# Optimization experiments

Hardware: AMD Instinct MI355X
Metric: run time of the kernel (lower is better)

## Reference

```python
import jax, jax.numpy as jnp
import numpy as np

D = 64      # hidden_dim
H = 4       # num_attention_heads
DH = D // H # head_dim
B = 64      # graphs per batch
SCALE = np.float32(np.sqrt(DH))


def _sage(x, edge, wl, bl, wr):
    # SAGEConv: lin_l(mean_j x_j) + lin_r(x_i); mean over incoming edges (dst = edge[1])
    src, dst = edge[0], edge[1]
    n = x.shape[0]
    agg = jax.ops.segment_sum(x[src], dst, num_segments=n)
    cnt = jax.ops.segment_sum(jnp.ones((edge.shape[1],), x.dtype), dst, num_segments=n)
    mean = agg / jnp.maximum(cnt, 1.0)[:, None]
    return mean @ wl + bl + x @ wr


def _cross_attn(xq, xk, w, b):
    # w: [3, D, D] stacked (Q, K, V) projections; b: [3, D]
    Q = (xq @ w[0] + b[0]).reshape(-1, H, DH)  # [Nq, H, DH]
    K = (xk @ w[1] + b[1]).reshape(-1, H, DH)  # [Nk, H, DH]
    V = (xk @ w[2] + b[2]).reshape(-1, H, DH)
    scores = jnp.einsum('qhd,khd->hqk', Q, K) / SCALE  # [H, Nq, Nk]
    wgt = jax.nn.softmax(scores, axis=-1)
    out = jnp.einsum('hqk,khd->qhd', wgt, V)
    return out.reshape(xq.shape[0], D)


def _segment_mean(x, seg, num):
    s = jax.ops.segment_sum(x, seg, num_segments=num)
    c = jax.ops.segment_sum(jnp.ones((x.shape[0],), x.dtype), seg, num_segments=num)
    return s / jnp.maximum(c, 1.0)[:, None]


def setup_inputs() -> dict:
    key = jax.random.key(0)
    ks = jax.random.split(key, 32)
    N_MOL, N_PROT, E_MOL, E_PROT = 2048, 8192, 32768, 131072
    MOL_IN, PROT_IN = 32, 64

    def lin(k, i, o, s=None):
        s = 1.0 / np.sqrt(i) if s is None else s
        return (jax.random.normal(k, (i, o), jnp.float32) * s)

    inp = {
        'x_mol': jax.random.normal(ks[0], (N_MOL, MOL_IN), jnp.float32),
        'x_prot': jax.random.normal(ks[1], (N_PROT, PROT_IN), jnp.float32),
        'm1_wl': lin(ks[2], MOL_IN, D), 'm1_bl': jnp.zeros((D,), jnp.float32), 'm1_wr': lin(ks[3], MOL_IN, D),
        'm2_wl': lin(ks[4], D, D), 'm2_bl': jnp.zeros((D,), jnp.float32), 'm2_wr': lin(ks[5], D, D),
        'p1_wl': lin(ks[6], PROT_IN, D), 'p1_bl': jnp.zeros((D,), jnp.float32), 'p1_wr': lin(ks[7], PROT_IN, D),
        'p2_wl': lin(ks[8], D, D), 'p2_bl': jnp.zeros((D,), jnp.float32), 'p2_wr': lin(ks[9], D, D),
        'amp_w': jax.random.normal(ks[10], (3, D, D), jnp.float32) / np.sqrt(D),
        'amp_b': jnp.zeros((3, D), jnp.float32),
        'apm_w': jax.random.normal(ks[11], (3, D, D), jnp.float32) / np.sqrt(D),
        'apm_b': jnp.zeros((3, D), jnp.float32),
        'fc1_w': lin(ks[12], 2 * D, D), 'fc1_b': jnp.zeros((D,), jnp.float32),
        'fc2_w': lin(ks[13], D, 1), 'fc2_b': jnp.zeros((1,), jnp.float32),
        'edge_mol': jax.random.randint(ks[14], (2, E_MOL), 0, N_MOL, jnp.int32),
        'edge_prot': jax.random.randint(ks[15], (2, E_PROT), 0, N_PROT, jnp.int32),
        'batch_mol': jnp.sort(jax.random.randint(ks[16], (N_MOL,), 0, B, jnp.int32)),
        'batch_prot': jnp.sort(jax.random.randint(ks[17], (N_PROT,), 0, B, jnp.int32)),
    }
    return inp


def reference(x_mol, x_prot,
              m1_wl, m1_bl, m1_wr, m2_wl, m2_bl, m2_wr,
              p1_wl, p1_bl, p1_wr, p2_wl, p2_bl, p2_wr,
              amp_w, amp_b, apm_w, apm_b,
              fc1_w, fc1_b, fc2_w, fc2_b,
              edge_mol, edge_prot, batch_mol, batch_prot):
    # two SAGE conv blocks per graph, ReLU after each (HeteroConv with one edge type)
    h_mol = jax.nn.relu(_sage(x_mol, edge_mol, m1_wl, m1_bl, m1_wr))
    h_mol = jax.nn.relu(_sage(h_mol, edge_mol, m2_wl, m2_bl, m2_wr))
    h_prot = jax.nn.relu(_sage(x_prot, edge_prot, p1_wl, p1_bl, p1_wr))
    h_prot = jax.nn.relu(_sage(h_prot, edge_prot, p2_wl, p2_bl, p2_wr))
    # cross attention (mol queries prot, prot queries mol) + residual
    h_mol_c = h_mol + _cross_attn(h_mol, h_prot, amp_w, amp_b)
    h_prot_c = h_prot + _cross_attn(h_prot, h_mol, apm_w, apm_b)
    # global mean pool per graph
    z_mol = _segment_mean(h_mol_c, batch_mol, B)    # [B, D]
    z_prot = _segment_mean(h_prot_c, batch_prot, B)  # [B, D]
    z = jnp.concatenate([z_mol, z_prot], axis=1)     # [B, 2D]
    x = jax.nn.relu(z @ fc1_w + fc1_b)
    out = jax.nn.sigmoid(x @ fc2_w + fc2_b)
    return out.squeeze(-1)  # [B]
```

## Files before the change

kernel.cpp:

```cpp
#include <hip/hip_runtime.h>
#include <math.h>

#define D 64
#define NB 64

typedef __attribute__((ext_vector_type(8))) short bf16x8;
typedef __attribute__((ext_vector_type(4))) float f32x4;
typedef __attribute__((ext_vector_type(16))) float f32x16;

#define M3(a, b, c) fmaxf(fmaxf((a), (b)), (c))

__device__ __forceinline__ unsigned short f2bf(float f) {
    unsigned u = __float_as_uint(f);
    u += 0x7FFF + ((u >> 16) & 1);
    return (unsigned short)(u >> 16);
}
__device__ __forceinline__ unsigned pk_bf16(float lo, float hi) {
    unsigned r;
    asm("v_cvt_pk_bf16_f32 %0, %1, %2" : "=v"(r) : "v"(lo), "v"(hi));
    return r;
}
__device__ __forceinline__ float fexp2(float x) {
    float r;
    asm("v_exp_f32 %0, %1" : "=v"(r) : "v"(x));
    return r;
}

__global__ void k_prep2(const int* __restrict__ em, int Em,
                        const int* __restrict__ ep, int Ep,
                        int* __restrict__ degm, int* __restrict__ degp,
                        const int* __restrict__ bm, int Nm, int* __restrict__ bsM,
                        const int* __restrict__ bp, int Np, int* __restrict__ bsP) {
    int i = blockIdx.x * blockDim.x + threadIdx.x;
    if (i < Em) atomicAdd(&degm[em[Em + i]], 1);
    int j = i - Em;
    if (j >= 0 && j < Ep) atomicAdd(&degp[ep[Ep + j]], 1);
    if (i < Nm) {
        int cur = bm[i];
        int prev = (i == 0) ? -1 : bm[i - 1];
        for (int b = prev + 1; b <= cur; ++b) bsM[b] = i;
        if (i == Nm - 1)
            for (int b = cur + 1; b <= NB; ++b) bsM[b] = Nm;
    }
    int j2 = i - Nm;
    if (j2 >= 0 && j2 < Np) {
        int cur = bp[j2];
        int prev = (j2 == 0) ? -1 : bp[j2 - 1];
        for (int b = prev + 1; b <= cur; ++b) bsP[b] = j2;
        if (j2 == Np - 1)
            for (int b = cur + 1; b <= NB; ++b) bsP[b] = Np;
    }
}

__global__ __launch_bounds__(256) void k_scan2(
        const int* __restrict__ degm, int Nm, int* __restrict__ rpm, int* __restrict__ curm,
        const int* __restrict__ degp, int Np, int* __restrict__ rpp, int* __restrict__ curp) {
    __shared__ int sdeg[8192];
    __shared__ int chunk[256];
    const int* deg = blockIdx.x ? degp : degm;
    int N = blockIdx.x ? Np : Nm;
    int* rowptr = blockIdx.x ? rpp : rpm;
    int* cursor = blockIdx.x ? curp : curm;
    int t = threadIdx.x;
    for (int i = t; i < N; i += 256) sdeg[i] = deg[i];
    __syncthreads();
    int C = (N + 255) / 256;
    int start = t * C;
    int sum = 0;
    for (int i = 0; i < C; ++i)
        if (start + i < N) sum += sdeg[start + i];
    chunk[t] = sum;
    __syncthreads();
    for (int ofs = 1; ofs < 256; ofs <<= 1) {
        int v = (t >= ofs) ? chunk[t - ofs] : 0;
        __syncthreads();
        chunk[t] += v;
        __syncthreads();
    }
    int base = (t == 0) ? 0 : chunk[t - 1];
    for (int i = 0; i < C && start + i < N; ++i) {
        rowptr[start + i] = base;
        cursor[start + i] = base;
        base += sdeg[start + i];
    }
    if (t == 255) rowptr[N] = base;
}

__global__ void k_scatter2(const int* __restrict__ em, int Em, int* __restrict__ curm,
                           int* __restrict__ csrm,
                           const int* __restrict__ ep, int Ep, int* __restrict__ curp,
                           int* __restrict__ csrp) {
    int i = blockIdx.x * blockDim.x + threadIdx.x;
    if (i < Em) {
        int s = em[i], d = em[Em + i];
        csrm[atomicAdd(&curm[d], 1)] = s;
    }
    int j = i - Em;
    if (j >= 0 && j < Ep) {
        int s = ep[j], d = ep[Ep + j];
        csrp[atomicAdd(&curp[d], 1)] = s;
    }
}

template<int FIN>
__device__ __forceinline__ void gsage_body(
        const float* __restrict__ x, const int* __restrict__ rowptr,
        const int* __restrict__ csr, int N,
        const float* __restrict__ wl, const float* __restrict__ bl,
        const float* __restrict__ wr, float* __restrict__ out,
        int blk, float* __restrict__ swl, float* __restrict__ swr,
        float* __restrict__ sagg, float* __restrict__ sx) {
    for (int i = threadIdx.x; i < FIN * D; i += 256) { swl[i] = wl[i]; swr[i] = wr[i]; }
    int w = threadIdx.x >> 6;
    int lane = threadIdx.x & 63;
    int r = blk * 4 + w;
    if (r < N) {
        int e0 = rowptr[r], e1 = rowptr[r + 1];
        float inv = 1.0f / fmaxf((float)(e1 - e0), 1.0f);
        if (FIN == 64) {
            float a0 = 0.f, a1 = 0.f, a2 = 0.f, a3 = 0.f;
            int e = e0;
            for (; e + 3 < e1; e += 4) {
                a0 += x[(size_t)csr[e] * FIN + lane];
                a1 += x[(size_t)csr[e + 1] * FIN + lane];
                a2 += x[(size_t)csr[e + 2] * FIN + lane];
                a3 += x[(size_t)csr[e + 3] * FIN + lane];
            }
            for (; e < e1; ++e) a0 += x[(size_t)csr[e] * FIN + lane];
            sagg[w * 64 + lane] = ((a0 + a1) + (a2 + a3)) * inv;
            sx[w * 64 + lane] = x[(size_t)r * FIN + lane];
        } else {
            int f = lane & 31, half = lane >> 5;
            float a = 0.f;
            for (int e = e0 + half; e < e1; e += 2)
                a += x[(size_t)csr[e] * FIN + f];
            a += __shfl_xor(a, 32);
            if (half == 0) {
                sagg[w * 64 + f] = a * inv;
                sx[w * 64 + f] = x[(size_t)r * FIN + f];
            }
        }
    }
    __syncthreads();
    if (r >= N) return;
    int c = lane;
    float acc = bl[c];
    #pragma unroll 8
    for (int k = 0; k < FIN; ++k) {
        acc += sagg[w * 64 + k] * swl[k * D + c];
        acc += sx[w * 64 + k] * swr[k * D + c];
    }
    out[(size_t)r * D + c] = fmaxf(acc, 0.0f);
}

template<int FA, int FB>
__global__ __launch_bounds__(256) void k_gsage2(
        const float* __restrict__ xA, const int* __restrict__ rpA,
        const int* __restrict__ csrA, int NA,
        const float* __restrict__ wlA, const float* __restrict__ blA,
        const float* __restrict__ wrA, float* __restrict__ outA,
        const float* __restrict__ xB, const int* __restrict__ rpB,
        const int* __restrict__ csrB, int NB_,
        const float* __restrict__ wlB, const float* __restrict__ blB,
        const float* __restrict__ wrB, float* __restrict__ outB) {
    __shared__ float swl[64 * 64];
    __shared__ float swr[64 * 64];
    __shared__ float sagg[4 * 64];
    __shared__ float sx[4 * 64];
    int bA = NA / 4;
    if ((int)blockIdx.x < bA)
        gsage_body<FA>(xA, rpA, csrA, NA, wlA, blA, wrA, outA, blockIdx.x, swl, swr, sagg, sx);
    else
        gsage_body<FB>(xB, rpB, csrB, NB_, wlB, blB, wrB, outB, blockIdx.x - bA, swl, swr, sagg, sx);
}

__global__ __launch_bounds__(256) void k_qkv2(
        const float* __restrict__ xA, int NA, const float* __restrict__ xB, int NB_,
        const float* __restrict__ amp_w, const float* __restrict__ amp_b,
        const float* __restrict__ apm_w, const float* __restrict__ apm_b, float qs,
        unsigned short* __restrict__ QA, unsigned short* __restrict__ KA, unsigned short* __restrict__ VA,
        unsigned short* __restrict__ QB, unsigned short* __restrict__ KB, unsigned short* __restrict__ VB) {
    __shared__ float sq[D * D], sk[D * D], sv[D * D], sx[16 * D];
    int bA = NA / 16;
    const float *x, *wq, *bq, *wk, *bk, *wv, *bv;
    unsigned short *oq, *ok, *ov;
    int blk;
    if ((int)blockIdx.x < bA) {
        x = xA; blk = blockIdx.x;
        wq = amp_w;        bq = amp_b;
        wk = apm_w + 4096; bk = apm_b + 64;
        wv = apm_w + 8192; bv = apm_b + 128;
        oq = QA; ok = KA; ov = VA;
    } else {
        x = xB; blk = blockIdx.x - bA;
        wq = apm_w;        bq = apm_b;
        wk = amp_w + 4096; bk = amp_b + 64;
        wv = amp_w + 8192; bv = amp_b + 128;
        oq = QB; ok = KB; ov = VB;
    }
    for (int i = threadIdx.x; i < D * D; i += 256) { sq[i] = wq[i]; sk[i] = wk[i]; sv[i] = wv[i]; }
    int rbase = blk * 16;
    for (int i = threadIdx.x; i < 16 * D; i += 256) sx[i] = x[(size_t)rbase * D + i];
    __syncthreads();
    int c = threadIdx.x & 63;
    int r0 = (threadIdx.x >> 6) * 4;
    for (int rr = 0; rr < 4; ++rr) {
        int r = r0 + rr;
        float aq = bq[c], ak = bk[c], av = bv[c];
        #pragma unroll 8
        for (int k = 0; k < D; ++k) {
            float xv = sx[r * D + k];
            aq += xv * sq[k * D + c];
            ak += xv * sk[k * D + c];
            av += xv * sv[k * D + c];
        }
        size_t o = (size_t)(rbase + r) * D + c;
        oq[o] = f2bf(aq * qs);
        ok[o] = f2bf(ak);
        ov[o] = f2bf(av);
    }
}

__global__ void k_transp2(const unsigned short* __restrict__ inM, unsigned short* __restrict__ outM, int Nm,
                          const unsigned short* __restrict__ inP, unsigned short* __restrict__ outP, int Np) {
    __shared__ unsigned short tile[64][72];
    int bm = Nm >> 6;
    const unsigned short* in; unsigned short* out; int N;
    int blk = blockIdx.x;
    if (blk < bm) { in = inM; out = outM; N = Nm; }
    else { blk -= bm; in = inP; out = outP; N = Np; }
    int t = threadIdx.x;
    int rbase = blk * 64;
    {
        int r = t >> 2, c0 = (t & 3) * 16;
        const uint4* src = (const uint4*)(in + (size_t)(rbase + r) * 64 + c0);
        uint4 a = src[0], b = src[1];
        *(uint4*)(&tile[r][c0]) = a;
        *(uint4*)(&tile[r][c0 + 8]) = b;
    }
    __syncthreads();
    {
        int c = t >> 2, r0 = (t & 3) * 16;
        union { uint2 v2[4]; unsigned short s[16]; } u;
        #pragma unroll
        for (int i = 0; i < 16; ++i) u.s[i] = tile[r0 + i][c];
        int key0 = rbase + r0;
        int kc = key0 & ~31;
        int b16 = key0 & 16;
        unsigned short* op = out + (size_t)c * N;
        const int gmap[4] = {0, 8, 4, 12};
        #pragma unroll
        for (int b = 0; b < 4; ++b)
            *(uint2*)(op + kc + b16 + gmap[b]) = u.v2[b];
    }
    if (t < 8) {
        uint4 ones;
        ones.x = ones.y = ones.z = ones.w = 0x3F803F80u;
        *(uint4*)(out + (size_t)64 * N + rbase + t * 8) = ones;
    }
}

#define MAXTREE(cm, s0, s1)                                                   \
    {                                                                         \
        float c0 = M3(s0[0], s0[1], s0[2]);                                   \
        float c1 = M3(s0[3], s0[4], s0[5]);                                   \
        float c2 = M3(s0[6], s0[7], s0[8]);                                   \
        float c3 = M3(s0[9], s0[10], s0[11]);                                 \
        float c4 = M3(s0[12], s0[13], s0[14]);                                \
        float c5 = M3(s0[15], s1[0], s1[1]);                                  \
        float c6 = M3(s1[2], s1[3], s1[4]);                                   \
        float c7 = M3(s1[5], s1[6], s1[7]);                                   \
        float c8 = M3(s1[8], s1[9], s1[10]);                                  \
        float c9 = M3(s1[11], s1[12], s1[13]);                                \
        float ca = fmaxf(s1[14], s1[15]);                                     \
        float d0 = M3(c0, c1, c2);                                            \
        float d1 = M3(c3, c4, c5);                                            \
        float d2 = M3(c6, c7, c8);                                            \
        float d3 = M3(c9, ca, d0);                                            \
        cm = M3(d1, d2, d3);                                                  \
    }

#define PVPACK(S, KB)                                                         \
    {                                                                         \
        union { unsigned u[4]; bf16x8 v; } f1, f2;                            \
        f1.u[0] = pk_bf16((S)[0], (S)[1]);   f1.u[1] = pk_bf16((S)[2], (S)[3]);  \
        f1.u[2] = pk_bf16((S)[4], (S)[5]);   f1.u[3] = pk_bf16((S)[6], (S)[7]);  \
        f2.u[0] = pk_bf16((S)[8], (S)[9]);   f2.u[1] = pk_bf16((S)[10], (S)[11]);\
        f2.u[2] = pk_bf16((S)[12], (S)[13]); f2.u[3] = pk_bf16((S)[14], (S)[15]);\
        bf16x8 vb0 = *(const bf16x8*)(vbase + (KB) + half * 8);               \
        bf16x8 vb1 = *(const bf16x8*)(vbase + (KB) + 16 + half * 8);          \
        __builtin_amdgcn_s_setprio(1);                                        \
        o = __builtin_amdgcn_mfma_f32_32x32x16_bf16(f1.v, vb0, o, 0, 0, 0);   \
        o = __builtin_amdgcn_mfma_f32_32x32x16_bf16(f2.v, vb1, o, 0, 0, 0);   \
        __builtin_amdgcn_s_setprio(0);                                        \
    }

__global__ __launch_bounds__(256) void k_attn5(
        const unsigned short* __restrict__ QmB, const unsigned short* __restrict__ KpB,
        const unsigned short* __restrict__ VpT, int Nm, int Np, int lsm,
        float* __restrict__ poM, float* __restrict__ pmM, float* __restrict__ plM,
        const unsigned short* __restrict__ QpB, const unsigned short* __restrict__ KmB,
        const unsigned short* __restrict__ VmT, int lsp,
        float* __restrict__ poP, float* __restrict__ pmP, float* __restrict__ plP) {
    const unsigned short *Q, *K, *Vt;
    int Nq, Nk, ls;
    float *po, *pm, *pl;
    if (blockIdx.y == 0) { Q = QmB; K = KpB; Vt = VpT; Nq = Nm; Nk = Np; ls = lsm; po = poM; pm = pmM; pl = plM; }
    else                 { Q = QpB; K = KmB; Vt = VmT; Nq = Np; Nk = Nm; ls = lsp; po = poP; pm = pmP; pl = plP; }
    int nqt = Nq >> 5;
    if ((int)blockIdx.x >= (nqt << ls)) return;
    const int qt = blockIdx.x >> ls;
    const int split = blockIdx.x & ((1 << ls) - 1);
    const int kchunk = Nk >> ls;
    const int h = threadIdx.x >> 6;
    const int lane = threadIdx.x & 63;
    const int cq = lane & 31;
    const int half = lane >> 5;
    const int h16 = h * 16;

    bf16x8 qb = *(const bf16x8*)(Q + ((size_t)(qt * 32 + cq) * D + h16 + half * 8));
    int drow = (cq < 16) ? (h16 + cq) : (cq == 16 ? 64 : h16 + 15);
    const unsigned short* vbase = Vt + (size_t)drow * Nk;

    f32x16 o, mC;
    #pragma unroll
    for (int i = 0; i < 16; ++i) { o[i] = 0.f; mC[i] = 0.f; }
    float m;

    const int kstart = split * kchunk;
    {
        const int kb = kstart;
        bf16x8 ka0 = *(const bf16x8*)(K + ((size_t)(kb + cq) * D + h16 + half * 8));
        bf16x8 ka1 = *(const bf16x8*)(K + ((size_t)(kb + 32 + cq) * D + h16 + half * 8));
        f32x16 s0 = __builtin_amdgcn_mfma_f32_32x32x16_bf16(ka0, qb, mC, 0, 0, 0);
        f32x16 s1 = __builtin_amdgcn_mfma_f32_32x32x16_bf16(ka1, qb, mC, 0, 0, 0);
        float cm;
        MAXTREE(cm, s0, s1);
        #pragma unroll
        for (int off = 1; off < 64; off <<= 1) cm = fmaxf(cm, __shfl_xor(cm, off));
        m = cm;
        #pragma unroll
        for (int i = 0; i < 16; ++i) {
            s0[i] = fexp2(s0[i] - m);
            s1[i] = fexp2(s1[i] - m);
            mC[i] = -m;
        }
        PVPACK(s0, kb)
        PVPACK(s1, kb + 32)
    }
    #pragma unroll 2
    for (int kb = kstart + 64; kb < kstart + kchunk; kb += 32) {
        bf16x8 ka = *(const bf16x8*)(K + ((size_t)(kb + cq) * D + h16 + half * 8));
        f32x16 s = __builtin_amdgcn_mfma_f32_32x32x16_bf16(ka, qb, mC, 0, 0, 0);
        #pragma unroll
        for (int i = 0; i < 16; ++i) s[i] = fexp2(s[i]);
        PVPACK(s, kb)
    }

    size_t pbase = (size_t)split * Nq + qt * 32;
    if (half == 0)
        pm[(pbase + cq) * 4 + h] = m;
    if (cq == 16) {
        #pragma unroll
        for (int r = 0; r < 16; ++r) {
            int qr = (r & 3) + 8 * (r >> 2) + 4 * half;
            pl[(pbase + qr) * 4 + h] = o[r];
        }
    }
    if (cq < 16) {
        #pragma unroll
        for (int r = 0; r < 16; ++r) {
            int qr = (r & 3) + 8 * (r >> 2) + 4 * half;
            po[(pbase + qr) * 64 + h16 + cq] = o[r];
        }
    }
}

template<int NS>
__device__ __forceinline__ void comb_body(
        const float* __restrict__ po, const float* __restrict__ pm,
        const float* __restrict__ pl, int Nq,
        const float* __restrict__ resid, float* __restrict__ outc, int i) {
    int q = i >> 4;
    int part = i & 15;
    int d0 = part * 4;
    int h = part >> 2;
    float pmv[NS], plv[NS];
    #pragma unroll
    for (int s = 0; s < NS; ++s) pmv[s] = pm[((size_t)s * Nq + q) * 4 + h];
    #pragma unroll
    for (int s = 0; s < NS; ++s) plv[s] = pl[((size_t)s * Nq + q) * 4 + h];
    float M = pmv[0];
    #pragma unroll
    for (int s = 1; s < NS; ++s) M = fmaxf(M, pmv[s]);
    float4 O = {0.f, 0.f, 0.f, 0.f};
    float L = 0.f;
    #pragma unroll
    for (int s = 0; s < NS; ++s) {
        float wgt = fexp2(pmv[s] - M);
        float4 pv = *(const float4*)(po + ((size_t)s * Nq + q) * 64 + d0);
        O.x += pv.x * wgt; O.y += pv.y * wgt; O.z += pv.z * wgt; O.w += pv.w * wgt;
        L += plv[s] * wgt;
    }
    float invL = 1.0f / L;
    float4 rv = *(const float4*)(resid + (size_t)q * 64 + d0);
    float4 res;
    res.x = rv.x + O.x * invL;
    res.y = rv.y + O.y * invL;
    res.z = rv.z + O.z * invL;
    res.w = rv.w + O.w * invL;
    *(float4*)(outc + (size_t)q * 64 + d0) = res;
}

template<int NSM, int NSP>
__global__ void k_comb2t(
        const float* __restrict__ poM, const float* __restrict__ pmM, const float* __restrict__ plM,
        int Nm, const float* __restrict__ residM, float* __restrict__ outM,
        const float* __restrict__ poP, const float* __restrict__ pmP, const float* __restrict__ plP,
        int Np, const float* __restrict__ residP, float* __restrict__ outP) {
    int idx = blockIdx.x * blockDim.x + threadIdx.x;
    int mtot = Nm * 16;
    if (idx < mtot)
        comb_body<NSM>(poM, pmM, plM, Nm, residM, outM, idx);
    else if (idx - mtot < Np * 16)
        comb_body<NSP>(poP, pmP, plP, Np, residP, outP, idx - mtot);
}

__global__ void k_comb2(
        const float* __restrict__ poM, const float* __restrict__ pmM, const float* __restrict__ plM,
        int nsM, int Nm, const float* __restrict__ residM, float* __restrict__ outM,
        const float* __restrict__ poP, const float* __restrict__ pmP, const float* __restrict__ plP,
        int nsP, int Np, const float* __restrict__ residP, float* __restrict__ outP) {
    int idx = blockIdx.x * blockDim.x + threadIdx.x;
    const float *po, *pm, *pl, *resid;
    float* outc;
    int ns, Nq, i;
    int mtot = Nm * 64;
    if (idx < mtot) {
        po = poM; pm = pmM; pl = plM; ns = nsM; Nq = Nm; resid = residM; outc = outM; i = idx;
    } else {
        i = idx - mtot;
        if (i >= Np * 64) return;
        po = poP; pm = pmP; pl = plP; ns = nsP; Nq = Np; resid = residP; outc = outP;
    }
    int q = i >> 6, d = i & 63, h = d >> 4;
    float M = -1e30f;
    for (int s = 0; s < ns; ++s)
        M = fmaxf(M, pm[((size_t)s * Nq + q) * 4 + h]);
    float O = 0.f, L = 0.f;
    for (int s = 0; s < ns; ++s) {
        float wgt = fexp2(pm[((size_t)s * Nq + q) * 4 + h] - M);
        O += po[((size_t)s * Nq + q) * 64 + d] * wgt;
        L += pl[((size_t)s * Nq + q) * 4 + h] * wgt;
    }
    outc[i] = resid[i] + O / L;
}

__global__ __launch_bounds__(256) void k_pool2(
        const float* __restrict__ hM, const int* __restrict__ bsM,
        const float* __restrict__ hP, const int* __restrict__ bsP,
        float* __restrict__ zsum, float* __restrict__ zcnt) {
    __shared__ float red[4][64];
    int b = blockIdx.x & 63;
    int isP = blockIdx.x >> 6;
    const float* h = isP ? hP : hM;
    const int* bs = isP ? bsP : bsM;
    int colOff = isP ? 64 : 0;
    int n0 = bs[b], n1 = bs[b + 1];
    int w = threadIdx.x >> 6, c = threadIdx.x & 63;
    float acc = 0.f;
    for (int n = n0 + w; n < n1; n += 4)
        acc += h[(size_t)n * 64 + c];
    red[w][c] = acc;
    __syncthreads();
    if (w == 0) {
        float s = (red[0][c] + red[1][c]) + (red[2][c] + red[3][c]);
        zsum[b * 128 + colOff + c] = s;
        if (c == 0) zcnt[b * 2 + isP] = (float)(n1 - n0);
    }
}

__global__ __launch_bounds__(256) void k_head2(
        const float* __restrict__ zsum, const float* __restrict__ zcnt,
        const float* __restrict__ fc1w, const float* __restrict__ fc1b,
        const float* __restrict__ fc2w, const float* __restrict__ fc2b,
        float* __restrict__ out) {
    int b = blockIdx.x * 4 + (threadIdx.x >> 6);
    int c = threadIdx.x & 63;
    float inv0 = 1.0f / fmaxf(zcnt[b * 2 + 0], 1.0f);
    float inv1 = 1.0f / fmaxf(zcnt[b * 2 + 1], 1.0f);
    float acc = fc1b[c];
    #pragma unroll 8
    for (int k = 0; k < 128; ++k) {
        float zv = zsum[b * 128 + k] * (k < 64 ? inv0 : inv1);
        acc += zv * fc1w[k * 64 + c];
    }
    float v = fmaxf(acc, 0.0f) * fc2w[c];
    #pragma unroll
    for (int off = 32; off > 0; off >>= 1) v += __shfl_xor(v, off);
    if (c == 0) out[b] = 1.0f / (1.0f + __expf(-(v + fc2b[0])));
}

extern "C" void kernel_launch(void* const* d_in, const int* in_sizes, int n_in,
                              void* d_out, int out_size, void* d_ws, size_t ws_size,
                              hipStream_t stream) {
    const float* x_mol  = (const float*)d_in[0];
    const float* x_prot = (const float*)d_in[1];
    const float* m1_wl = (const float*)d_in[2];
    const float* m1_bl = (const float*)d_in[3];
    const float* m1_wr = (const float*)d_in[4];
    const float* m2_wl = (const float*)d_in[5];
    const float* m2_bl = (const float*)d_in[6];
    const float* m2_wr = (const float*)d_in[7];
    const float* p1_wl = (const float*)d_in[8];
    const float* p1_bl = (const float*)d_in[9];
    const float* p1_wr = (const float*)d_in[10];
    const float* p2_wl = (const float*)d_in[11];
    const float* p2_bl = (const float*)d_in[12];
    const float* p2_wr = (const float*)d_in[13];
    const float* amp_w = (const float*)d_in[14];
    const float* amp_b = (const float*)d_in[15];
    const float* apm_w = (const float*)d_in[16];
    const float* apm_b = (const float*)d_in[17];
    const float* fc1_w = (const float*)d_in[18];
    const float* fc1_b = (const float*)d_in[19];
    const float* fc2_w = (const float*)d_in[20];
    const float* fc2_b = (const float*)d_in[21];
    const int* edge_mol  = (const int*)d_in[22];
    const int* edge_prot = (const int*)d_in[23];
    const int* batch_mol  = (const int*)d_in[24];
    const int* batch_prot = (const int*)d_in[25];
    float* out = (float*)d_out;

    const int N_MOL  = in_sizes[0] / 32;
    const int N_PROT = in_sizes[1] / 64;
    const int E_MOL  = in_sizes[22] / 2;
    const int E_PROT = in_sizes[23] / 2;

    char* base = (char*)d_ws;
    size_t off = 0;
    auto alloc = [&](size_t bytes) -> void* {
        void* p = base + off;
        off = (off + bytes + 255) & ~(size_t)255;
        return p;
    };
    float* h_mol1   = (float*)alloc((size_t)N_MOL * D * sizeof(float));
    float* h_mol2   = (float*)alloc((size_t)N_MOL * D * sizeof(float));
    float* h_prot1  = (float*)alloc((size_t)N_PROT * D * sizeof(float));
    float* h_prot2  = (float*)alloc((size_t)N_PROT * D * sizeof(float));
    float* h_mol_c  = (float*)alloc((size_t)N_MOL * D * sizeof(float));
    float* h_prot_c = (float*)alloc((size_t)N_PROT * D * sizeof(float));
    float* zsum     = (float*)alloc((NB * 128 + NB * 2) * sizeof(float));
    float* zcnt     = zsum + NB * 128;
    unsigned short* Qm_b = (unsigned short*)alloc((size_t)N_MOL * D * 2);
    unsigned short* Km_b = (unsigned short*)alloc((size_t)N_MOL * D * 2);
    unsigned short* Vm_b = (unsigned short*)alloc((size_t)N_MOL * D * 2);
    unsigned short* Vm_t = (unsigned short*)alloc((size_t)N_MOL * (D + 1) * 2);
    unsigned short* Qp_b = (unsigned short*)alloc((size_t)N_PROT * D * 2);
    unsigned short* Kp_b = (unsigned short*)alloc((size_t)N_PROT * D * 2);
    unsigned short* Vp_b = (unsigned short*)alloc((size_t)N_PROT * D * 2);
    unsigned short* Vp_t = (unsigned short*)alloc((size_t)N_PROT * (D + 1) * 2);
    int* deg      = (int*)alloc(((size_t)N_MOL + N_PROT) * sizeof(int));
    int* deg_m    = deg;
    int* deg_p    = deg + N_MOL;
    int* rp_m     = (int*)alloc(((size_t)N_MOL + 1) * sizeof(int));
    int* cur_m    = (int*)alloc((size_t)N_MOL * sizeof(int));
    int* csr_m    = (int*)alloc((size_t)E_MOL * sizeof(int));
    int* rp_p     = (int*)alloc(((size_t)N_PROT + 1) * sizeof(int));
    int* cur_p    = (int*)alloc((size_t)N_PROT * sizeof(int));
    int* csr_p    = (int*)alloc((size_t)E_PROT * sizeof(int));
    int* bsM      = (int*)alloc((NB + 1) * sizeof(int));
    int* bsP      = (int*)alloc((NB + 1) * sizeof(int));

    int nsm = 16; while (nsm > 1 && (N_PROT % (64 * nsm))) nsm >>= 1;
    int nsp = 4;  while (nsp > 1 && (N_MOL % (64 * nsp)))  nsp >>= 1;
    int lsm = 31 - __builtin_clz(nsm);
    int lsp = 31 - __builtin_clz(nsp);
    float* poM = (float*)alloc((size_t)nsm * N_MOL * 64 * sizeof(float));
    float* pmM = (float*)alloc((size_t)nsm * N_MOL * 4 * sizeof(float));
    float* plM = (float*)alloc((size_t)nsm * N_MOL * 4 * sizeof(float));
    float* poP = (float*)alloc((size_t)nsp * N_PROT * 64 * sizeof(float));
    float* pmP = (float*)alloc((size_t)nsp * N_PROT * 4 * sizeof(float));
    float* plP = (float*)alloc((size_t)nsp * N_PROT * 4 * sizeof(float));

    const int BLK = 256;
    dim3 blk(BLK);
    const float QS = 0.25f * 1.4426950408889634f;

    hipMemsetAsync(deg, 0, ((size_t)N_MOL + N_PROT) * sizeof(int), stream);
    int Etot = E_MOL + E_PROT;
    k_prep2<<<(Etot + BLK - 1) / BLK, blk, 0, stream>>>(
        edge_mol, E_MOL, edge_prot, E_PROT, deg_m, deg_p,
        batch_mol, N_MOL, bsM, batch_prot, N_PROT, bsP);
    k_scan2<<<2, blk, 0, stream>>>(deg_m, N_MOL, rp_m, cur_m, deg_p, N_PROT, rp_p, cur_p);
    k_scatter2<<<(Etot + BLK - 1) / BLK, blk, 0, stream>>>(edge_mol, E_MOL, cur_m, csr_m,
                                                           edge_prot, E_PROT, cur_p, csr_p);

    k_gsage2<32, 64><<<N_MOL / 4 + N_PROT / 4, blk, 0, stream>>>(
        x_mol,  rp_m, csr_m, N_MOL,  m1_wl, m1_bl, m1_wr, h_mol1,
        x_prot, rp_p, csr_p, N_PROT, p1_wl, p1_bl, p1_wr, h_prot1);
    k_gsage2<64, 64><<<N_MOL / 4 + N_PROT / 4, blk, 0, stream>>>(
        h_mol1,  rp_m, csr_m, N_MOL,  m2_wl, m2_bl, m2_wr, h_mol2,
        h_prot1, rp_p, csr_p, N_PROT, p2_wl, p2_bl, p2_wr, h_prot2);

    k_qkv2<<<N_MOL / 16 + N_PROT / 16, blk, 0, stream>>>(
        h_mol2, N_MOL, h_prot2, N_PROT, amp_w, amp_b, apm_w, apm_b, QS,
        Qm_b, Km_b, Vm_b, Qp_b, Kp_b, Vp_b);

    k_transp2<<<N_MOL / 64 + N_PROT / 64, blk, 0, stream>>>(Vm_b, Vm_t, N_MOL, Vp_b, Vp_t, N_PROT);

    int gxm = (N_MOL / 32) * nsm;
    int gxp = (N_PROT / 32) * nsp;
    int gx = gxm > gxp ? gxm : gxp;
    k_attn5<<<dim3(gx, 2), blk, 0, stream>>>(
        Qm_b, Kp_b, Vp_t, N_MOL, N_PROT, lsm, poM, pmM, plM,
        Qp_b, Km_b, Vm_t, lsp, poP, pmP, plP);

    if (nsm == 16 && nsp == 4) {
        int tot = (N_MOL + N_PROT) * 16;
        k_comb2t<16, 4><<<(tot + BLK - 1) / BLK, blk, 0, stream>>>(
            poM, pmM, plM, N_MOL, h_mol2, h_mol_c,
            poP, pmP, plP, N_PROT, h_prot2, h_prot_c);
    } else {
        k_comb2<<<((N_MOL + N_PROT) * 64 + BLK - 1) / BLK, blk, 0, stream>>>(
            poM, pmM, plM, nsm, N_MOL, h_mol2, h_mol_c,
            poP, pmP, plP, nsp, N_PROT, h_prot2, h_prot_c);
    }

    k_pool2<<<128, blk, 0, stream>>>(h_mol_c, bsM, h_prot_c, bsP, zsum, zcnt);

    k_head2<<<16, blk, 0, stream>>>(zsum, zcnt, fc1_w, fc1_b, fc2_w, fc2_b, out);
}
```

Before: 174.3 us.

## Add lazy online-softmax rescaling and pack two query tiles per 512-thread block

The attention kernel now handles two 32-row query tiles per block using 512 threads, and processes keys 64 at a time. The old loop used the max from the first chunk only. The new loop computes a per-chunk max and rescales the accumulator only when some score exceeds the running max by more than a threshold, which is lazy online-softmax rescaling. This adds a max-tree and a wave vote per iteration in exchange for numerical robustness and larger blocks. It may raise register pressure or reduce occupancy.

```diff
diff --git a/kernel.cpp b/kernel.cpp
--- a/kernel.cpp
+++ b/kernel.cpp
@@ -295,7 +295,7 @@
         __builtin_amdgcn_s_setprio(0);                                        \
     }
 
-__global__ __launch_bounds__(256) void k_attn5(
+__global__ __launch_bounds__(512) void k_attn6(
         const unsigned short* __restrict__ QmB, const unsigned short* __restrict__ KpB,
         const unsigned short* __restrict__ VpT, int Nm, int Np, int lsm,
         float* __restrict__ poM, float* __restrict__ pmM, float* __restrict__ plM,
@@ -307,12 +307,14 @@
     float *po, *pm, *pl;
     if (blockIdx.y == 0) { Q = QmB; K = KpB; Vt = VpT; Nq = Nm; Nk = Np; ls = lsm; po = poM; pm = pmM; pl = plM; }
     else                 { Q = QpB; K = KmB; Vt = VmT; Nq = Np; Nk = Nm; ls = lsp; po = poP; pm = pmP; pl = plP; }
-    int nqt = Nq >> 5;
-    if ((int)blockIdx.x >= (nqt << ls)) return;
-    const int qt = blockIdx.x >> ls;
+    int npair = Nq >> 6;
+    if ((int)blockIdx.x >= (npair << ls)) return;
+    const int qpair = blockIdx.x >> ls;
     const int split = blockIdx.x & ((1 << ls) - 1);
     const int kchunk = Nk >> ls;
-    const int h = threadIdx.x >> 6;
+    const int w = threadIdx.x >> 6;
+    const int h = w & 3;
+    const int qt = qpair * 2 + (w >> 2);
     const int lane = threadIdx.x & 63;
     const int cq = lane & 31;
     const int half = lane >> 5;
@@ -348,13 +350,30 @@
         PVPACK(s0, kb)
         PVPACK(s1, kb + 32)
     }
-    #pragma unroll 2
-    for (int kb = kstart + 64; kb < kstart + kchunk; kb += 32) {
-        bf16x8 ka = *(const bf16x8*)(K + ((size_t)(kb + cq) * D + h16 + half * 8));
-        f32x16 s = __builtin_amdgcn_mfma_f32_32x32x16_bf16(ka, qb, mC, 0, 0, 0);
+    for (int kb = kstart + 64; kb < kstart + kchunk; kb += 64) {
+        bf16x8 ka0 = *(const bf16x8*)(K + ((size_t)(kb + cq) * D + h16 + half * 8));
+        bf16x8 ka1 = *(const bf16x8*)(K + ((size_t)(kb + 32 + cq) * D + h16 + half * 8));
+        f32x16 s0 = __builtin_amdgcn_mfma_f32_32x32x16_bf16(ka0, qb, mC, 0, 0, 0);
+        f32x16 s1 = __builtin_amdgcn_mfma_f32_32x32x16_bf16(ka1, qb, mC, 0, 0, 0);
+        float cm;
+        MAXTREE(cm, s0, s1);
+        if (__any(cm > 8.f)) {
+            float cw = cm;
+            #pragma unroll
+            for (int off = 1; off < 64; off <<= 1) cw = fmaxf(cw, __shfl_xor(cw, off));
+            float nm = fmaxf(m + cw, m);
+            float sc = fexp2(m - nm);
+            #pragma unroll
+            for (int i = 0; i < 16; ++i) o[i] *= sc;
+            float dl = nm - m;
+            #pragma unroll
+            for (int i = 0; i < 16; ++i) { s0[i] -= dl; s1[i] -= dl; mC[i] = -nm; }
+            m = nm;
+        }
         #pragma unroll
-        for (int i = 0; i < 16; ++i) s[i] = fexp2(s[i]);
-        PVPACK(s, kb)
+        for (int i = 0; i < 16; ++i) { s0[i] = fexp2(s0[i]); s1[i] = fexp2(s1[i]); }
+        PVPACK(s0, kb)
+        PVPACK(s1, kb + 32)
     }
 
     size_t pbase = (size_t)split * Nq + qt * 32;
@@ -609,10 +628,10 @@
 
     k_transp2<<<N_MOL / 64 + N_PROT / 64, blk, 0, stream>>>(Vm_b, Vm_t, N_MOL, Vp_b, Vp_t, N_PROT);
 
-    int gxm = (N_MOL / 32) * nsm;
-    int gxp = (N_PROT / 32) * nsp;
+    int gxm = (N_MOL / 64) * nsm;
+    int gxp = (N_PROT / 64) * nsp;
     int gx = gxm > gxp ? gxm : gxp;
-    k_attn5<<<dim3(gx, 2), blk, 0, stream>>>(
+    k_attn6<<<dim3(gx, 2), dim3(512), 0, stream>>>(
         Qm_b, Kp_b, Vp_t, N_MOL, N_PROT, lsm, poM, pmM, plM,
         Qp_b, Km_b, Vm_t, lsp, poP, pmP, plP);
 
```

Measured after the change: 171.9 us. No clear change (-1.4%).
